# Performance work log

Measured on AMD Instinct MI355X. Metric: run time of the kernel, lower is better.

Reference implementation:

```python
import jax, jax.numpy as jnp
import numpy as np

EPS = 1e-6
SLOPE = 0.01  # torch LeakyReLU / VNLeakyReLU default negative_slope
B = 1024      # number of graphs (segments)
N, S, V, H = 120000, 256, 64, 64


def _vn(W, x):
    # VNLinear: channel-mixing linear on (N, C, 3) vector features, W: (O, C)
    return jnp.einsum('oc,ncd->nod', W, x)


def _gv_linear(Wv1, Wv2, Ws, Wg, bg, sca, vec):
    # GVLinear: vec -> hidden vec, concat |vec| with sca, gate out_vec by sigmoid(out_sca)
    vi = _vn(Wv1, vec)                                   # (N, Hid, 3)
    vnorm = jnp.linalg.norm(vi, axis=-1)                 # (N, Hid)
    out_sca = jnp.concatenate([vnorm, sca], axis=-1) @ Ws.T   # (N, out_sca)
    out_vec = _vn(Wv2, vi)                               # (N, out_vec, 3)
    gate = jax.nn.sigmoid(out_sca @ Wg.T + bg)[..., None]
    return out_sca, gate * out_vec


def _vn_lrelu(Wd, x):
    # VNLeakyReLU: direction-gated leaky relu on vector channels
    d = _vn(Wd, x)
    dot = jnp.sum(x * d, axis=-1, keepdims=True)
    dsq = jnp.sum(d * d, axis=-1, keepdims=True)
    mask = (dot >= 0).astype(x.dtype)
    proj = x - (dot / (dsq + EPS)) * d
    return SLOPE * x + (1.0 - SLOPE) * (mask * x + (1.0 - mask) * proj)


def _lrelu(x):
    return jnp.where(x >= 0, x, SLOPE * x)


def setup_inputs() -> dict:
    key = jax.random.key(0)
    ks = jax.random.split(key, 40)
    g = lambda i, shape, s=1.0: jax.random.normal(ks[i], shape, dtype=jnp.float32) * s
    w = 0.06  # ~1/sqrt(fan_in) for fan_in 256-320
    inp = {
        'h_sca': g(0, (N, S)),
        'h_vec': g(1, (N, V, 3)),
        'pos_context': g(2, (N, 3), 3.0),
        'time_embed': g(3, (100, S), 0.05),
        # att_net: GVPerceptronVN(256,64 -> 256,64)
        'att1_Wv1': g(4, (H, V), 0.12), 'att1_Wv2': g(5, (H, H), 0.12),
        'att1_Ws': g(6, (S, S + H), w), 'att1_Wg': g(7, (H, S), w), 'att1_bg': g(8, (H,), 0.01),
        'att1_Wd': g(9, (H, H), 0.12),
        # att_net: GVLinear(256,64 -> 1,1), dim_hid = max(64,1) = 64
        'att2_Wv1': g(10, (H, H), 0.12), 'att2_Wv2': g(11, (1, H), 0.12),
        'att2_Ws': g(12, (1, S + H), w), 'att2_Wg': g(13, (1, 1), 0.5), 'att2_bg': g(14, (1,), 0.01),
        # net: GVPerceptronVN(256,64 -> 256,64)
        'net1_Wv1': g(15, (H, V), 0.12), 'net1_Wv2': g(16, (H, H), 0.12),
        'net1_Ws': g(17, (S, S + H), w), 'net1_Wg': g(18, (H, S), w), 'net1_bg': g(19, (H,), 0.01),
        'net1_Wd': g(20, (H, H), 0.12),
        # net: GVLinear(256,64 -> 256,64)
        'net2_Wv1': g(21, (H, H), 0.12), 'net2_Wv2': g(22, (S - (S - V), H), 0.12).reshape(V, H),
        'net2_Ws': g(23, (S, S + H), w), 'net2_Wg': g(24, (V, S), w), 'net2_bg': g(25, (V,), 0.01),
        't': 17,
        'batch_id': jnp.sort(jax.random.randint(ks[30], (N,), 0, B)),
    }
    return inp


def reference(h_sca, h_vec, pos_context, time_embed,
              att1_Wv1, att1_Wv2, att1_Ws, att1_Wg, att1_bg, att1_Wd,
              att2_Wv1, att2_Wv2, att2_Ws, att2_Wg, att2_bg,
              net1_Wv1, net1_Wv2, net1_Ws, net1_Wg, net1_bg, net1_Wd,
              net2_Wv1, net2_Wv2, net2_Ws, net2_Wg, net2_bg,
              t, batch_id):
    sca = h_sca + time_embed[t]          # same timestep embedding broadcast to all N nodes
    vec = h_vec

    # attention branch: GVPerceptronVN -> GVLinear(...,1,1), keep scalar output
    s, v = _gv_linear(att1_Wv1, att1_Wv2, att1_Ws, att1_Wg, att1_bg, sca, vec)
    s, v = _lrelu(s), _vn_lrelu(att1_Wd, v)
    att, _ = _gv_linear(att2_Wv1, att2_Wv2, att2_Ws, att2_Wg, att2_bg, s, v)  # (N,1)

    # feature branch: GVPerceptronVN -> GVLinear(...,in_sca,in_vec)
    s2, v2 = _gv_linear(net1_Wv1, net1_Wv2, net1_Ws, net1_Wg, net1_bg, sca, vec)
    s2, v2 = _lrelu(s2), _vn_lrelu(net1_Wd, v2)
    fs, fv = _gv_linear(net2_Wv1, net2_Wv2, net2_Ws, net2_Wg, net2_bg, s2, v2)

    # scatter_softmax over batch_id segments
    m = jax.ops.segment_max(att, batch_id, num_segments=B)
    e = jnp.exp(att - m[batch_id])
    z = jax.ops.segment_sum(e, batch_id, num_segments=B)
    w = e / z[batch_id]                  # (N,1)

    pos_focal = jax.ops.segment_sum(w * pos_context, batch_id, num_segments=B)   # (B,3)
    feat_focal = jax.ops.segment_sum(w * fs, batch_id, num_segments=B)           # (B,256)
    vec_focal = jax.ops.segment_sum(w[:, :, None] * fv, batch_id, num_segments=B)  # (B,64,3)
    return feat_focal, vec_focal, pos_focal
```

## Files before the change

### kernel.cpp

```cpp
#include <hip/hip_runtime.h>
#include <hip/hip_bf16.h>
#include <math.h>

#define NN 120000
#define NT 32
#define TPB 512
#define NBLK (NN / NT)
#define BSEG 1024

typedef __attribute__((ext_vector_type(8))) short short8;
typedef __attribute__((ext_vector_type(16))) float floatx16;

#define OFF_A1_WV1 0
#define OFF_A1_WV2 4096
#define OFF_A1_WS  8192
#define OFF_A1_WG  90112
#define OFF_A1_WD  106496
#define OFF_A2_WV1 110592
#define OFF_N1_WV1 114688
#define OFF_N1_WV2 118784
#define OFF_N1_WS  122880
#define OFF_N1_WG  204800
#define OFF_N1_WD  221184
#define OFF_N2_WV1 225280
#define OFF_N2_WV2 229376
#define OFF_N2_WS  233472
#define OFF_N2_WG  315392
#define W_TOTAL    331776

__device__ __forceinline__ unsigned short f2bf(float x) {
  __hip_bfloat16 b = __float2bfloat16(x);
  return __builtin_bit_cast(unsigned short, b);
}
__device__ __forceinline__ unsigned int f2bf2(float lo, float hi) {
  return (unsigned int)f2bf(lo) | ((unsigned int)f2bf(hi) << 16);
}
__device__ __forceinline__ float bf2f(unsigned short h) {
  return __uint_as_float(((unsigned int)h) << 16);
}
__device__ __forceinline__ float bflo(unsigned int u) { return __uint_as_float(u << 16); }
__device__ __forceinline__ float bfhi(unsigned int u) { return __uint_as_float(u & 0xffff0000u); }

struct P {
  const float *h_sca, *h_vec, *pos, *te;
  const float *a1_bg, *n1_bg, *n2_bg, *a2_Ws;
  const int *t, *bid;
  const unsigned short* wb;
  float *att, *w, *out;
};


struct CvtP { const float* src[15]; unsigned short* dst; };

__global__ __launch_bounds__(256) void cvt_kernel(CvtP c) {
  const int sizes[15] = {4096, 4096, 81920, 16384, 4096, 4096,
                         4096, 4096, 81920, 16384, 4096,
                         4096, 4096, 81920, 16384};
  int idx = blockIdx.x * 256 + threadIdx.x;
  if (idx >= W_TOTAL) return;
  int seg = 0, off = 0;
  while (idx - off >= sizes[seg]) { off += sizes[seg]; ++seg; }
  c.dst[idx] = f2bf(c.src[seg][idx - off]);
}


__device__ __forceinline__ void stage(const P& p, unsigned short* sS, unsigned short* sV,
                                      const float* te_row, int node0, int tid) {
  int i = tid >> 4, j = tid & 15;
  {
    int c0 = j * 16;
    const float4* src = (const float4*)&p.h_sca[(node0 + i) * 256 + c0];
    const float4* te4 = (const float4*)&te_row[c0];
    float4 a0 = src[0], b0 = te4[0];
    float4 a1 = src[1], b1 = te4[1];
    float4 a2 = src[2], b2 = te4[2];
    float4 a3 = src[3], b3 = te4[3];
    uint4 o0 = make_uint4(f2bf2(a0.x + b0.x, a0.y + b0.y), f2bf2(a0.z + b0.z, a0.w + b0.w),
                          f2bf2(a1.x + b1.x, a1.y + b1.y), f2bf2(a1.z + b1.z, a1.w + b1.w));
    uint4 o1 = make_uint4(f2bf2(a2.x + b2.x, a2.y + b2.y), f2bf2(a2.z + b2.z, a2.w + b2.w),
                          f2bf2(a3.x + b3.x, a3.y + b3.y), f2bf2(a3.z + b3.z, a3.w + b3.w));
    *(uint4*)&sS[i * 264 + c0] = o0;
    *(uint4*)&sS[i * 264 + c0 + 8] = o1;
  }
  {
    int c0 = j * 4;
    const float4* src = (const float4*)&p.h_vec[(node0 + i) * 192 + c0 * 3];
    float4 v0 = src[0], v1 = src[1], v2 = src[2];
    int b = (i * 3) * 72 + c0;
    *(uint2*)&sV[b]       = make_uint2(f2bf2(v0.x, v0.w), f2bf2(v1.z, v2.y));
    *(uint2*)&sV[b + 72]  = make_uint2(f2bf2(v0.y, v1.x), f2bf2(v1.w, v2.z));
    *(uint2*)&sV[b + 144] = make_uint2(f2bf2(v0.z, v1.y), f2bf2(v2.x, v2.w));
  }
}

__device__ __forceinline__ void big_gemm(const unsigned short* __restrict__ Wb,
                                         const unsigned short* sVN,
                                         const unsigned short* sX,
                                         unsigned short* sDst,
                                         int wid, int lane) {
  const int m = lane & 31, h = lane >> 5;
  const int n0 = wid * 32;
  const unsigned short* wrow = Wb + (n0 + m) * 320 + h * 8;
  floatx16 acc0 = {}, acc1 = {};
#pragma unroll
  for (int k = 0; k < 20; k += 2) {
    short8 a0, a1;
    if (k < 4)     a0 = *(const short8*)&sVN[m * 72 + k * 16 + h * 8];
    else           a0 = *(const short8*)&sX[m * 264 + (k - 4) * 16 + h * 8];
    if (k + 1 < 4) a1 = *(const short8*)&sVN[m * 72 + (k + 1) * 16 + h * 8];
    else           a1 = *(const short8*)&sX[m * 264 + (k - 3) * 16 + h * 8];
    short8 b0 = *(const short8*)&wrow[k * 16];
    short8 b1 = *(const short8*)&wrow[k * 16 + 16];
    acc0 = __builtin_amdgcn_mfma_f32_32x32x16_bf16(a0, b0, acc0, 0, 0, 0);
    acc1 = __builtin_amdgcn_mfma_f32_32x32x16_bf16(a1, b1, acc1, 0, 0, 0);
  }
  __syncthreads();
#pragma unroll
  for (int r = 0; r < 16; ++r) {
    int row = (r & 3) + 8 * (r >> 2) + 4 * h;
    sDst[row * 264 + n0 + m] = f2bf(acc0[r] + acc1[r]);
  }
}

__device__ __forceinline__ void gate_gemm(const unsigned short* __restrict__ Wg,
                                          const float* __restrict__ bg,
                                          const unsigned short* sX,
                                          unsigned short* sG, int wid, int lane) {
  const int m = lane & 31, h = lane >> 5;
  const int n0 = wid * 32;
  const unsigned short* wrow = Wg + (n0 + m) * 256 + h * 8;
  floatx16 acc0 = {}, acc1 = {};
#pragma unroll
  for (int k = 0; k < 16; k += 2) {
    short8 a0 = *(const short8*)&sX[m * 264 + k * 16 + h * 8];
    short8 a1 = *(const short8*)&sX[m * 264 + k * 16 + 16 + h * 8];
    short8 b0 = *(const short8*)&wrow[k * 16];
    short8 b1 = *(const short8*)&wrow[k * 16 + 16];
    acc0 = __builtin_amdgcn_mfma_f32_32x32x16_bf16(a0, b0, acc0, 0, 0, 0);
    acc1 = __builtin_amdgcn_mfma_f32_32x32x16_bf16(a1, b1, acc1, 0, 0, 0);
  }
  float bb = bg[n0 + m];
#pragma unroll
  for (int r = 0; r < 16; ++r) {
    int i = (r & 3) + 8 * (r >> 2) + 4 * h;
    float v = acc0[r] + acc1[r] + bb;
    sG[i * 64 + n0 + m] = f2bf(__builtin_amdgcn_rcpf(1.f + __expf(-v)));
  }
}

__device__ __forceinline__ void vecmm(const unsigned short* __restrict__ Wb,
                                      const unsigned short* sSrc,
                                      unsigned short* sDst,
                                      int wid, int lane) {
  if (wid >= 6) return;
  const int m = lane & 31, h = lane >> 5;
  const int nd0 = (wid >> 1) * 32, o0 = (wid & 1) * 32;
  const unsigned short* wrow = Wb + (o0 + m) * 64 + h * 8;
  short8 b0 = *(const short8*)&wrow[0];
  short8 b1 = *(const short8*)&wrow[16];
  short8 b2 = *(const short8*)&wrow[32];
  short8 b3 = *(const short8*)&wrow[48];
  floatx16 acc = {};
#pragma unroll
  for (int k0 = 0; k0 < 64; k0 += 16) {
    short8 a = *(const short8*)&sSrc[(nd0 + m) * 72 + k0 + h * 8];
    short8 b = (k0 == 0) ? b0 : (k0 == 16) ? b1 : (k0 == 32) ? b2 : b3;
    acc = __builtin_amdgcn_mfma_f32_32x32x16_bf16(a, b, acc, 0, 0, 0);
  }
#pragma unroll
  for (int r = 0; r < 16; ++r) {
    int nd = nd0 + (r & 3) + 8 * (r >> 2) + 4 * h;
    sDst[nd * 72 + o0 + m] = f2bf(acc[r]);
  }
}

__device__ __forceinline__ void vnorm(const unsigned short* sV, unsigned short* sVN, int tid) {
  if (tid >= 256) return;
  int i = tid >> 3, c0 = (tid & 7) * 8;
  int b = (i * 3) * 72 + c0;
  short8 vx = *(const short8*)&sV[b];
  short8 vy = *(const short8*)&sV[b + 72];
  short8 vz = *(const short8*)&sV[b + 144];
  unsigned int o[4];
#pragma unroll
  for (int q = 0; q < 4; ++q) {
    float x0 = bf2f((unsigned short)vx[2 * q]),     y0 = bf2f((unsigned short)vy[2 * q]),     z0 = bf2f((unsigned short)vz[2 * q]);
    float x1 = bf2f((unsigned short)vx[2 * q + 1]), y1 = bf2f((unsigned short)vy[2 * q + 1]), z1 = bf2f((unsigned short)vz[2 * q + 1]);
    o[q] = f2bf2(sqrtf(x0 * x0 + y0 * y0 + z0 * z0), sqrtf(x1 * x1 + y1 * y1 + z1 * z1));
  }
  *(uint4*)&sVN[i * 72 + c0] = make_uint4(o[0], o[1], o[2], o[3]);
}

__device__ __forceinline__ void gatemul(unsigned short* sVx, const unsigned short* sG, int tid) {
  if (tid >= 256) return;
  int i = tid >> 3, c0 = (tid & 7) * 8;
  short8 g = *(const short8*)&sG[i * 64 + c0];
  float gf[8];
#pragma unroll
  for (int j = 0; j < 8; ++j) gf[j] = bf2f((unsigned short)g[j]);
  int b = (i * 3) * 72 + c0;
#pragma unroll
  for (int d = 0; d < 3; ++d) {
    short8 v = *(const short8*)&sVx[b + d * 72];
    unsigned int o[4];
#pragma unroll
    for (int q = 0; q < 4; ++q)
      o[q] = f2bf2(bf2f((unsigned short)v[2 * q]) * gf[2 * q],
                   bf2f((unsigned short)v[2 * q + 1]) * gf[2 * q + 1]);
    *(uint4*)&sVx[b + d * 72] = make_uint4(o[0], o[1], o[2], o[3]);
  }
}

__device__ __forceinline__ void vn_lrelu(unsigned short* sVx, const unsigned short* sVd, int tid) {
  if (tid >= 256) return;
  int i = tid >> 3, c0 = (tid & 7) * 8;
  int b = (i * 3) * 72 + c0;
  short8 x0 = *(const short8*)&sVx[b];
  short8 x1 = *(const short8*)&sVx[b + 72];
  short8 x2 = *(const short8*)&sVx[b + 144];
  short8 d0 = *(const short8*)&sVd[b];
  short8 d1 = *(const short8*)&sVd[b + 72];
  short8 d2 = *(const short8*)&sVd[b + 144];
  float rx[8], ry[8], rz[8];
#pragma unroll
  for (int j = 0; j < 8; ++j) {
    float a0 = bf2f((unsigned short)x0[j]), a1 = bf2f((unsigned short)x1[j]), a2 = bf2f((unsigned short)x2[j]);
    float e0 = bf2f((unsigned short)d0[j]), e1 = bf2f((unsigned short)d1[j]), e2 = bf2f((unsigned short)d2[j]);
    float dot = a0 * e0 + a1 * e1 + a2 * e2;
    float dsq = e0 * e0 + e1 * e1 + e2 * e2;
    float f = dot >= 0.f ? 0.f : 0.99f * dot * __builtin_amdgcn_rcpf(dsq + 1e-6f);
    rx[j] = a0 - f * e0; ry[j] = a1 - f * e1; rz[j] = a2 - f * e2;
  }
  unsigned int ox[4], oy[4], oz[4];
#pragma unroll
  for (int q = 0; q < 4; ++q) {
    ox[q] = f2bf2(rx[2 * q], rx[2 * q + 1]);
    oy[q] = f2bf2(ry[2 * q], ry[2 * q + 1]);
    oz[q] = f2bf2(rz[2 * q], rz[2 * q + 1]);
  }
  *(uint4*)&sVx[b]       = make_uint4(ox[0], ox[1], ox[2], ox[3]);
  *(uint4*)&sVx[b + 72]  = make_uint4(oy[0], oy[1], oy[2], oy[3]);
  *(uint4*)&sVx[b + 144] = make_uint4(oz[0], oz[1], oz[2], oz[3]);
}

__device__ __forceinline__ void lrelu_vec(unsigned short* sS, int u, int nthr) {
  for (int cc = u; cc < NT * 32; cc += nthr) {
    int i = cc >> 5, off = (cc & 31) * 8;
    short8 v = *(short8*)&sS[i * 264 + off];
    unsigned int o[4];
#pragma unroll
    for (int q = 0; q < 4; ++q) {
      float a = bf2f((unsigned short)v[2 * q]);
      float b = bf2f((unsigned short)v[2 * q + 1]);
      a = a >= 0.f ? a : 0.01f * a;
      b = b >= 0.f ? b : 0.01f * b;
      o[q] = f2bf2(a, b);
    }
    *(uint4*)&sS[i * 264 + off] = make_uint4(o[0], o[1], o[2], o[3]);
  }
}

__device__ __forceinline__ float* out_addr(float* out, int b, int f) {
  if (f < 256) return out + b * 256 + f;
  if (f < 448) return out + 1024 * 256 + b * 192 + (f - 256);
  return out + 1024 * 256 + 1024 * 192 + b * 3 + (f - 448);
}


__global__ __launch_bounds__(TPB, 6) void att_kernel(P p) {
  __shared__ unsigned short sS[NT * 264];
  __shared__ unsigned short sVA[96 * 72], sVB[96 * 72];
  __shared__ unsigned short sGN[2304];
  unsigned short* sVN = sGN;
  unsigned short* sG = sGN;
  int tid = threadIdx.x, wid = tid >> 6, lane = tid & 63;
  int node0 = blockIdx.x * NT;
  const unsigned short* wb = p.wb;

  stage(p, sS, sVA, p.te + p.t[0] * 256, node0, tid); __syncthreads();
  vecmm(wb + OFF_A1_WV1, sVA, sVB, wid, lane); __syncthreads();
  vnorm(sVB, sVN, tid); __syncthreads();
  big_gemm(wb + OFF_A1_WS, sVN, sS, sS, wid, lane); __syncthreads();
  if (wid < 2) gate_gemm(wb + OFF_A1_WG, p.a1_bg, sS, sG, wid, lane);
  else vecmm(wb + OFF_A1_WV2, sVB, sVA, wid - 2, lane);
  __syncthreads();
  gatemul(sVA, sG, tid); __syncthreads();
  vecmm(wb + OFF_A1_WD, sVA, sVB, wid, lane); __syncthreads();
  vn_lrelu(sVA, sVB, tid); __syncthreads();
  vecmm(wb + OFF_A2_WV1, sVA, sVB, wid, lane); __syncthreads();

  int i = tid >> 4, j = tid & 15;
  float part = 0.f;
  {
    int c0 = j * 4;
    uint2 wx = *(const uint2*)&sVB[(i * 3 + 0) * 72 + c0];
    uint2 wy = *(const uint2*)&sVB[(i * 3 + 1) * 72 + c0];
    uint2 wz = *(const uint2*)&sVB[(i * 3 + 2) * 72 + c0];
    float4 ws = *(const float4*)&p.a2_Ws[c0];
    float n0 = sqrtf(bflo(wx.x) * bflo(wx.x) + bflo(wy.x) * bflo(wy.x) + bflo(wz.x) * bflo(wz.x));
    float n1 = sqrtf(bfhi(wx.x) * bfhi(wx.x) + bfhi(wy.x) * bfhi(wy.x) + bfhi(wz.x) * bfhi(wz.x));
    float n2 = sqrtf(bflo(wx.y) * bflo(wx.y) + bflo(wy.y) * bflo(wy.y) + bflo(wz.y) * bflo(wz.y));
    float n3 = sqrtf(bfhi(wx.y) * bfhi(wx.y) + bfhi(wy.y) * bfhi(wy.y) + bfhi(wz.y) * bfhi(wz.y));
    part = fmaf(ws.x, n0, part);
    part = fmaf(ws.y, n1, part);
    part = fmaf(ws.z, n2, part);
    part = fmaf(ws.w, n3, part);
  }
  {
    int k0 = j * 16;
    short8 s0 = *(const short8*)&sS[i * 264 + k0];
    short8 s1 = *(const short8*)&sS[i * 264 + k0 + 8];
    const float4* wp = (const float4*)&p.a2_Ws[64 + k0];
#pragma unroll
    for (int q = 0; q < 4; ++q) {
      float4 w4 = wp[q];
      float vv[4];
#pragma unroll
      for (int e = 0; e < 4; ++e) {
        short raw = (q < 2) ? ((q == 0) ? s0[e] : s0[4 + e]) : ((q == 2) ? s1[e] : s1[4 + e]);
        float x = bf2f((unsigned short)raw);
        vv[e] = x >= 0.f ? x : 0.01f * x;
      }
      part = fmaf(w4.x, vv[0], part);
      part = fmaf(w4.y, vv[1], part);
      part = fmaf(w4.z, vv[2], part);
      part = fmaf(w4.w, vv[3], part);
    }
  }
  part += __shfl_down(part, 8, 16);
  part += __shfl_down(part, 4, 16);
  part += __shfl_down(part, 2, 16);
  part += __shfl_down(part, 1, 16);
  if (j == 0) p.att[node0 + i] = part;
}


__global__ __launch_bounds__(256) void softmax_kernel(const float* __restrict__ att,
                                                      const int* __restrict__ bid,
                                                      float* __restrict__ w) {
  __shared__ float red[256];
  __shared__ float s_m, s_z;
  int b = blockIdx.x, tid = threadIdx.x;
  int lo = 0, hi = NN;
  while (lo < hi) { int mid = (lo + hi) >> 1; if (bid[mid] < b) lo = mid + 1; else hi = mid; }
  int start = lo;
  hi = NN;
  while (lo < hi) { int mid = (lo + hi) >> 1; if (bid[mid] < b + 1) lo = mid + 1; else hi = mid; }
  int end = lo;

  float m = -1e30f;
  for (int i = start + tid; i < end; i += 256) m = fmaxf(m, att[i]);
  red[tid] = m; __syncthreads();
  for (int s = 128; s > 0; s >>= 1) { if (tid < s) red[tid] = fmaxf(red[tid], red[tid + s]); __syncthreads(); }
  if (tid == 0) s_m = red[0];
  __syncthreads();
  m = s_m;
  float z = 0.f;
  for (int i = start + tid; i < end; i += 256) z += __expf(att[i] - m);
  red[tid] = z; __syncthreads();
  for (int s = 128; s > 0; s >>= 1) { if (tid < s) red[tid] += red[tid + s]; __syncthreads(); }
  if (tid == 0) s_z = red[0];
  __syncthreads();
  float inv = 1.f / s_z;
  for (int i = start + tid; i < end; i += 256) w[i] = __expf(att[i] - m) * inv;
}


__global__ __launch_bounds__(TPB, 6) void net_kernel(P p) {
  __shared__ unsigned short sS[NT * 264];
  __shared__ unsigned short sVA[96 * 72], sVB[96 * 72];
  __shared__ unsigned short sGN[2304];
  __shared__ float s_w[NT];
  __shared__ float s_pos[NT * 3];
  __shared__ int s_bid[NT];
  unsigned short* sVN = sGN;
  unsigned short* sG = sGN;
  int tid = threadIdx.x, wid = tid >> 6, lane = tid & 63;
  int node0 = blockIdx.x * NT;
  const unsigned short* wb = p.wb;

  stage(p, sS, sVA, p.te + p.t[0] * 256, node0, tid); __syncthreads();
  vecmm(wb + OFF_N1_WV1, sVA, sVB, wid, lane);
  if (wid >= 6) {
    int u = tid - 384;
    if (u < NT) { s_w[u] = p.w[node0 + u]; s_bid[u] = p.bid[node0 + u]; }
    for (int v = u; v < NT * 3; v += 128) s_pos[v] = p.pos[node0 * 3 + v];
  }
  __syncthreads();
  vnorm(sVB, sVN, tid); __syncthreads();
  big_gemm(wb + OFF_N1_WS, sVN, sS, sS, wid, lane); __syncthreads();
  if (wid < 2) gate_gemm(wb + OFF_N1_WG, p.n1_bg, sS, sG, wid, lane);
  else vecmm(wb + OFF_N1_WV2, sVB, sVA, wid - 2, lane);
  __syncthreads();
  if (tid < 256) gatemul(sVA, sG, tid);
  else lrelu_vec(sS, tid - 256, 256);
  __syncthreads();
  vecmm(wb + OFF_N1_WD, sVA, sVB, wid, lane); __syncthreads();
  vn_lrelu(sVA, sVB, tid); __syncthreads();
  vecmm(wb + OFF_N2_WV1, sVA, sVB, wid, lane); __syncthreads();
  vnorm(sVB, sVN, tid); __syncthreads();
  big_gemm(wb + OFF_N2_WS, sVN, sS, sS, wid, lane); __syncthreads();
  if (wid < 2) gate_gemm(wb + OFF_N2_WG, p.n2_bg, sS, sG, wid, lane);
  else vecmm(wb + OFF_N2_WV2, sVB, sVA, wid - 2, lane);
  __syncthreads();

  if (tid < 451) {
    int f = tid;
    float acc = 0.f;
    int cur = s_bid[0];
    int c = 0, d = 0;
    if (f >= 256 && f < 448) { int r = f - 256; c = r / 3; d = r - c * 3; }
    for (int i2 = 0; i2 < NT; ++i2) {
      int sg = s_bid[i2];
      if (sg != cur) { atomicAdd(out_addr(p.out, cur, f), acc); acc = 0.f; cur = sg; }
      float val;
      if (f < 256) val = bf2f(sS[i2 * 264 + f]);
      else if (f < 448)
        val = bf2f(sVA[(i2 * 3 + d) * 72 + c]) * bf2f(sG[i2 * 64 + c]);
      else val = s_pos[i2 * 3 + (f - 448)];
      acc = fmaf(s_w[i2], val, acc);
    }
    atomicAdd(out_addr(p.out, cur, f), acc);
  }
}


extern "C" void kernel_launch(void* const* d_in, const int* in_sizes, int n_in,
                              void* d_out, int out_size, void* d_ws, size_t ws_size,
                              hipStream_t stream) {
  float* ws = (float*)d_ws;
  unsigned short* wb = (unsigned short*)(ws + 2 * NN);

  CvtP c;
  c.src[0]  = (const float*)d_in[4];
  c.src[1]  = (const float*)d_in[5];
  c.src[2]  = (const float*)d_in[6];
  c.src[3]  = (const float*)d_in[7];
  c.src[4]  = (const float*)d_in[9];
  c.src[5]  = (const float*)d_in[10];
  c.src[6]  = (const float*)d_in[15];
  c.src[7]  = (const float*)d_in[16];
  c.src[8]  = (const float*)d_in[17];
  c.src[9]  = (const float*)d_in[18];
  c.src[10] = (const float*)d_in[20];
  c.src[11] = (const float*)d_in[21];
  c.src[12] = (const float*)d_in[22];
  c.src[13] = (const float*)d_in[23];
  c.src[14] = (const float*)d_in[24];
  c.dst = wb;

  P p;
  p.h_sca = (const float*)d_in[0];
  p.h_vec = (const float*)d_in[1];
  p.pos   = (const float*)d_in[2];
  p.te    = (const float*)d_in[3];
  p.a1_bg = (const float*)d_in[8];
  p.a2_Ws = (const float*)d_in[12];
  p.n1_bg = (const float*)d_in[19];
  p.n2_bg = (const float*)d_in[25];
  p.t   = (const int*)d_in[26];
  p.bid = (const int*)d_in[27];
  p.wb  = wb;
  p.att = ws;
  p.w   = ws + NN;
  p.out = (float*)d_out;

  hipMemsetAsync(d_out, 0, (size_t)out_size * sizeof(float), stream);
  cvt_kernel<<<(W_TOTAL + 255) / 256, 256, 0, stream>>>(c);
  att_kernel<<<NBLK, TPB, 0, stream>>>(p);
  softmax_kernel<<<BSEG, 256, 0, stream>>>(p.att, p.bid, p.w);
  net_kernel<<<NBLK, TPB, 0, stream>>>(p);
}
```

Baseline: 658.8 us.

## Halve node tile to 16 nodes with 256-thread blocks and remap MFMA work

Shrinks each block from 32 nodes and 512 threads to 16 nodes and 256 threads. The GEMM helpers are reworked to match. big_gemm now has each wave compute two 32-column output tiles with one shared A operand. vecmm is renumbered into jobs so each wave covers two jobs, and rows past the valid count are clamped on read and masked on write. The aim is to cut LDS per block and raise occupancy or scheduling granularity. The cost is that the 32x32 MFMA tiles are now half filled with padding rows, and weights are streamed twice as often per node.

```diff
diff --git a/kernel.cpp b/kernel.cpp
--- a/kernel.cpp
+++ b/kernel.cpp
@@ -3,8 +3,8 @@
 #include <math.h>
 
 #define NN 120000
-#define NT 32
-#define TPB 512
+#define NT 16
+#define TPB 256
 #define NBLK (NN / NT)
 #define BSEG 1024
 
@@ -99,26 +99,29 @@
                                          unsigned short* sDst,
                                          int wid, int lane) {
   const int m = lane & 31, h = lane >> 5;
+  const int mr = m < NT ? m : (NT - 1);
   const int n0 = wid * 32;
-  const unsigned short* wrow = Wb + (n0 + m) * 320 + h * 8;
-  floatx16 acc0 = {}, acc1 = {};
-#pragma unroll
-  for (int k = 0; k < 20; k += 2) {
-    short8 a0, a1;
-    if (k < 4)     a0 = *(const short8*)&sVN[m * 72 + k * 16 + h * 8];
-    else           a0 = *(const short8*)&sX[m * 264 + (k - 4) * 16 + h * 8];
-    if (k + 1 < 4) a1 = *(const short8*)&sVN[m * 72 + (k + 1) * 16 + h * 8];
-    else           a1 = *(const short8*)&sX[m * 264 + (k - 3) * 16 + h * 8];
-    short8 b0 = *(const short8*)&wrow[k * 16];
-    short8 b1 = *(const short8*)&wrow[k * 16 + 16];
-    acc0 = __builtin_amdgcn_mfma_f32_32x32x16_bf16(a0, b0, acc0, 0, 0, 0);
-    acc1 = __builtin_amdgcn_mfma_f32_32x32x16_bf16(a1, b1, acc1, 0, 0, 0);
+  const unsigned short* wrowA = Wb + (n0 + m) * 320 + h * 8;
+  const unsigned short* wrowB = Wb + (n0 + 128 + m) * 320 + h * 8;
+  floatx16 accA = {}, accB = {};
+#pragma unroll
+  for (int k = 0; k < 20; ++k) {
+    short8 a;
+    if (k < 4) a = *(const short8*)&sVN[mr * 72 + k * 16 + h * 8];
+    else       a = *(const short8*)&sX[mr * 264 + (k - 4) * 16 + h * 8];
+    short8 bA = *(const short8*)&wrowA[k * 16];
+    short8 bB = *(const short8*)&wrowB[k * 16];
+    accA = __builtin_amdgcn_mfma_f32_32x32x16_bf16(a, bA, accA, 0, 0, 0);
+    accB = __builtin_amdgcn_mfma_f32_32x32x16_bf16(a, bB, accB, 0, 0, 0);
   }
   __syncthreads();
 #pragma unroll
   for (int r = 0; r < 16; ++r) {
     int row = (r & 3) + 8 * (r >> 2) + 4 * h;
-    sDst[row * 264 + n0 + m] = f2bf(acc0[r] + acc1[r]);
+    if (row < NT) {
+      sDst[row * 264 + n0 + m]       = f2bf(accA[r]);
+      sDst[row * 264 + n0 + 128 + m] = f2bf(accB[r]);
+    }
   }
 }
 
@@ -127,13 +130,14 @@
                                           const unsigned short* sX,
                                           unsigned short* sG, int wid, int lane) {
   const int m = lane & 31, h = lane >> 5;
+  const int mr = m < NT ? m : (NT - 1);
   const int n0 = wid * 32;
   const unsigned short* wrow = Wg + (n0 + m) * 256 + h * 8;
   floatx16 acc0 = {}, acc1 = {};
 #pragma unroll
   for (int k = 0; k < 16; k += 2) {
-    short8 a0 = *(const short8*)&sX[m * 264 + k * 16 + h * 8];
-    short8 a1 = *(const short8*)&sX[m * 264 + k * 16 + 16 + h * 8];
+    short8 a0 = *(const short8*)&sX[mr * 264 + k * 16 + h * 8];
+    short8 a1 = *(const short8*)&sX[mr * 264 + k * 16 + 16 + h * 8];
     short8 b0 = *(const short8*)&wrow[k * 16];
     short8 b1 = *(const short8*)&wrow[k * 16 + 16];
     acc0 = __builtin_amdgcn_mfma_f32_32x32x16_bf16(a0, b0, acc0, 0, 0, 0);
@@ -143,18 +147,21 @@
 #pragma unroll
   for (int r = 0; r < 16; ++r) {
     int i = (r & 3) + 8 * (r >> 2) + 4 * h;
-    float v = acc0[r] + acc1[r] + bb;
-    sG[i * 64 + n0 + m] = f2bf(__builtin_amdgcn_rcpf(1.f + __expf(-v)));
+    if (i < NT) {
+      float v = acc0[r] + acc1[r] + bb;
+      sG[i * 64 + n0 + m] = f2bf(__builtin_amdgcn_rcpf(1.f + __expf(-v)));
+    }
   }
 }
 
 __device__ __forceinline__ void vecmm(const unsigned short* __restrict__ Wb,
                                       const unsigned short* sSrc,
                                       unsigned short* sDst,
-                                      int wid, int lane) {
-  if (wid >= 6) return;
+                                      int job, int lane) {
+  if (job >= 4) return;
   const int m = lane & 31, h = lane >> 5;
-  const int nd0 = (wid >> 1) * 32, o0 = (wid & 1) * 32;
+  const int nd0 = (job >> 1) * 32, o0 = (job & 1) * 32;
+  int rr = nd0 + m; if (rr > 47) rr = 47;
   const unsigned short* wrow = Wb + (o0 + m) * 64 + h * 8;
   short8 b0 = *(const short8*)&wrow[0];
   short8 b1 = *(const short8*)&wrow[16];
@@ -163,19 +170,19 @@
   floatx16 acc = {};
 #pragma unroll
   for (int k0 = 0; k0 < 64; k0 += 16) {
-    short8 a = *(const short8*)&sSrc[(nd0 + m) * 72 + k0 + h * 8];
+    short8 a = *(const short8*)&sSrc[rr * 72 + k0 + h * 8];
     short8 b = (k0 == 0) ? b0 : (k0 == 16) ? b1 : (k0 == 32) ? b2 : b3;
     acc = __builtin_amdgcn_mfma_f32_32x32x16_bf16(a, b, acc, 0, 0, 0);
   }
 #pragma unroll
   for (int r = 0; r < 16; ++r) {
     int nd = nd0 + (r & 3) + 8 * (r >> 2) + 4 * h;
-    sDst[nd * 72 + o0 + m] = f2bf(acc[r]);
+    if (nd < 48) sDst[nd * 72 + o0 + m] = f2bf(acc[r]);
   }
 }
 
 __device__ __forceinline__ void vnorm(const unsigned short* sV, unsigned short* sVN, int tid) {
-  if (tid >= 256) return;
+  if (tid >= NT * 8) return;
   int i = tid >> 3, c0 = (tid & 7) * 8;
   int b = (i * 3) * 72 + c0;
   short8 vx = *(const short8*)&sV[b];
@@ -192,7 +199,7 @@
 }
 
 __device__ __forceinline__ void gatemul(unsigned short* sVx, const unsigned short* sG, int tid) {
-  if (tid >= 256) return;
+  if (tid >= NT * 8) return;
   int i = tid >> 3, c0 = (tid & 7) * 8;
   short8 g = *(const short8*)&sG[i * 64 + c0];
   float gf[8];
@@ -212,7 +219,7 @@
 }
 
 __device__ __forceinline__ void vn_lrelu(unsigned short* sVx, const unsigned short* sVd, int tid) {
-  if (tid >= 256) return;
+  if (tid >= NT * 8) return;
   int i = tid >> 3, c0 = (tid & 7) * 8;
   int b = (i * 3) * 72 + c0;
   short8 x0 = *(const short8*)&sVx[b];
@@ -269,8 +276,8 @@
 
 __global__ __launch_bounds__(TPB, 6) void att_kernel(P p) {
   __shared__ unsigned short sS[NT * 264];
-  __shared__ unsigned short sVA[96 * 72], sVB[96 * 72];
-  __shared__ unsigned short sGN[2304];
+  __shared__ unsigned short sVA[48 * 72], sVB[48 * 72];
+  __shared__ unsigned short sGN[NT * 72];
   unsigned short* sVN = sGN;
   unsigned short* sG = sGN;
   int tid = threadIdx.x, wid = tid >> 6, lane = tid & 63;
@@ -282,7 +289,8 @@
   vnorm(sVB, sVN, tid); __syncthreads();
   big_gemm(wb + OFF_A1_WS, sVN, sS, sS, wid, lane); __syncthreads();
   if (wid < 2) gate_gemm(wb + OFF_A1_WG, p.a1_bg, sS, sG, wid, lane);
-  else vecmm(wb + OFF_A1_WV2, sVB, sVA, wid - 2, lane);
+  else { vecmm(wb + OFF_A1_WV2, sVB, sVA, wid - 2, lane);
+         vecmm(wb + OFF_A1_WV2, sVB, sVA, wid, lane); }
   __syncthreads();
   gatemul(sVA, sG, tid); __syncthreads();
   vecmm(wb + OFF_A1_WD, sVA, sVB, wid, lane); __syncthreads();
@@ -368,8 +376,8 @@
 
 __global__ __launch_bounds__(TPB, 6) void net_kernel(P p) {
   __shared__ unsigned short sS[NT * 264];
-  __shared__ unsigned short sVA[96 * 72], sVB[96 * 72];
-  __shared__ unsigned short sGN[2304];
+  __shared__ unsigned short sVA[48 * 72], sVB[48 * 72];
+  __shared__ unsigned short sGN[NT * 72];
   __shared__ float s_w[NT];
   __shared__ float s_pos[NT * 3];
   __shared__ int s_bid[NT];
@@ -379,21 +387,19 @@
   int node0 = blockIdx.x * NT;
   const unsigned short* wb = p.wb;
 
-  stage(p, sS, sVA, p.te + p.t[0] * 256, node0, tid); __syncthreads();
-  vecmm(wb + OFF_N1_WV1, sVA, sVB, wid, lane);
-  if (wid >= 6) {
-    int u = tid - 384;
-    if (u < NT) { s_w[u] = p.w[node0 + u]; s_bid[u] = p.bid[node0 + u]; }
-    for (int v = u; v < NT * 3; v += 128) s_pos[v] = p.pos[node0 * 3 + v];
-  }
-  __syncthreads();
+  stage(p, sS, sVA, p.te + p.t[0] * 256, node0, tid);
+  if (tid < NT) { s_w[tid] = p.w[node0 + tid]; s_bid[tid] = p.bid[node0 + tid]; }
+  if (tid < NT * 3) s_pos[tid] = p.pos[node0 * 3 + tid];
+  __syncthreads();
+  vecmm(wb + OFF_N1_WV1, sVA, sVB, wid, lane); __syncthreads();
   vnorm(sVB, sVN, tid); __syncthreads();
   big_gemm(wb + OFF_N1_WS, sVN, sS, sS, wid, lane); __syncthreads();
   if (wid < 2) gate_gemm(wb + OFF_N1_WG, p.n1_bg, sS, sG, wid, lane);
-  else vecmm(wb + OFF_N1_WV2, sVB, sVA, wid - 2, lane);
-  __syncthreads();
-  if (tid < 256) gatemul(sVA, sG, tid);
-  else lrelu_vec(sS, tid - 256, 256);
+  else { vecmm(wb + OFF_N1_WV2, sVB, sVA, wid - 2, lane);
+         vecmm(wb + OFF_N1_WV2, sVB, sVA, wid, lane); }
+  __syncthreads();
+  if (tid < NT * 8) gatemul(sVA, sG, tid);
+  else lrelu_vec(sS, tid - NT * 8, TPB - NT * 8);
   __syncthreads();
   vecmm(wb + OFF_N1_WD, sVA, sVB, wid, lane); __syncthreads();
   vn_lrelu(sVA, sVB, tid); __syncthreads();
@@ -401,11 +407,14 @@
   vnorm(sVB, sVN, tid); __syncthreads();
   big_gemm(wb + OFF_N2_WS, sVN, sS, sS, wid, lane); __syncthreads();
   if (wid < 2) gate_gemm(wb + OFF_N2_WG, p.n2_bg, sS, sG, wid, lane);
-  else vecmm(wb + OFF_N2_WV2, sVB, sVA, wid - 2, lane);
-  __syncthreads();
-
-  if (tid < 451) {
-    int f = tid;
+  else { vecmm(wb + OFF_N2_WV2, sVB, sVA, wid - 2, lane);
+         vecmm(wb + OFF_N2_WV2, sVB, sVA, wid, lane); }
+  __syncthreads();
+
+#pragma unroll
+  for (int half = 0; half < 2; ++half) {
+    int f = tid + half * 256;
+    if (f >= 451) break;
     float acc = 0.f;
     int cur = s_bid[0];
     int c = 0, d = 0;
```

New measurement: 935.3 us. 1.42x slower.
